# Kernel tuning notes

Measured on AMD Instinct MI355X. Metric: run time of the kernel, lower is better.

Reference implementation:

```python
import jax, jax.numpy as jnp
import numpy as np

N, D, H, HID, QK, V, PSI_HID, OUT = 100000, 128, 8, 256, 64, 64, 256, 128


def _p(key, shape, fan_in):
    return jax.random.normal(key, shape, dtype=jnp.float32) / np.sqrt(fan_in)


def setup_inputs() -> dict:
    key = jax.random.key(0)
    ks = jax.random.split(key, 16)
    coordinates = jax.random.normal(ks[0], (N, D), dtype=jnp.float32)
    mask = jnp.ones((N,), dtype=jnp.float32)
    inp = {"coordinates": coordinates, "mask": mask}
    # per-head 2-layer MLPs for q, k, v, stacked along head axis
    for name, outd, k0, k1 in (("q", QK, 1, 2), ("k", QK, 3, 4), ("v", V, 5, 6)):
        inp[f"W{name}0"] = _p(ks[k0], (H, D, HID), D)
        inp[f"b{name}0"] = jnp.zeros((H, HID), dtype=jnp.float32)
        inp[f"W{name}1"] = _p(ks[k1], (H, HID, outd), HID)
        inp[f"b{name}1"] = jnp.zeros((H, outd), dtype=jnp.float32)
    # psi MLP: concat(H*V) -> PSI_HID -> OUT
    inp["Wp0"] = _p(ks[7], (H * V, PSI_HID), H * V)
    inp["bp0"] = jnp.zeros((PSI_HID,), dtype=jnp.float32)
    inp["Wp1"] = _p(ks[8], (PSI_HID, OUT), PSI_HID)
    inp["bp1"] = jnp.zeros((OUT,), dtype=jnp.float32)
    return inp


def _mlp_heads(x, W0, b0, W1, b1):
    # x: [N, D]; W0: [H, D, M]; W1: [H, M, O] -> [H, N, O]
    h = jax.nn.relu(jnp.einsum("nd,hdm->hnm", x, W0) + b0[:, None, :])
    return jnp.einsum("hnm,hmo->hno", h, W1) + b1[:, None, :]


def _phi(x):
    return jax.nn.elu(x) + 1.0  # positive kernel feature map


def reference(coordinates, mask, Wq0, bq0, Wq1, bq1, Wk0, bk0, Wk1, bk1,
              Wv0, bv0, Wv1, bv1, Wp0, bp0, Wp1, bp1):
    m = mask[None, :, None]
    q = _mlp_heads(coordinates, Wq0, bq0, Wq1, bq1) * m  # [H, N, QK]
    k = _mlp_heads(coordinates, Wk0, bk0, Wk1, bk1) * m  # [H, N, QK]
    v = _mlp_heads(coordinates, Wv0, bv0, Wv1, bv1) * m  # [H, N, V]
    qk = _phi(q)
    kk = _phi(k)
    kv = jnp.einsum("hnk,hnv->hkv", kk, v)          # global phi(K)^T V
    sum_k = jnp.sum(kk, axis=1)                      # [H, QK]
    num = jnp.einsum("hnk,hkv->hnv", qk, kv)         # [H, N, V]
    den = jnp.einsum("hnk,hk->hn", qk, sum_k)[..., None]
    den = jnp.where(den == 0, 1e-6, den)
    heads = num / den                                # [H, N, V]
    cat = jnp.transpose(heads, (1, 0, 2)).reshape(coordinates.shape[0], -1)
    h = jax.nn.relu(cat @ Wp0 + bp0)
    out = (h @ Wp1 + bp1) * mask[:, None]
    return out
```

## Files before the change

kernel.cpp:

```cpp
#include <hip/hip_runtime.h>
#include <hip/hip_bf16.h>
#include <math.h>

#define NPTS 100000
#define NPAD 100352
#define NHALF 50176
#define RPB 3136
#define HIDST 40
#define KVST 264

typedef __bf16 bf16x8 __attribute__((ext_vector_type(8)));
typedef __bf16 bf16x4 __attribute__((ext_vector_type(4)));
typedef float f32x4 __attribute__((ext_vector_type(4)));

#define MFMA16(a,b,c) __builtin_amdgcn_mfma_f32_16x16x32_bf16((a),(b),(c),0,0,0)
#define SW(row) (((row)&7)<<3)

__global__ void k_prep_w(const float* __restrict__ Wq0, const float* __restrict__ Wk0,
                         const float* __restrict__ Wv0, const float* __restrict__ Wq1,
                         const float* __restrict__ Wk1, const float* __restrict__ Wv1,
                         const float* __restrict__ Wp0, const float* __restrict__ Wp1,
                         __bf16* __restrict__ W0t, __bf16* __restrict__ W1t,
                         __bf16* __restrict__ Wp0t, __bf16* __restrict__ Wp1t) {
  for (int i = blockIdx.x * 256 + threadIdx.x; i < 1343488; i += gridDim.x * 256) {
    if (i < 786432) {
      int g = i >> 15, j = i & 32767;
      int mat = g >> 3, h = g & 7, mcol = j >> 7, k = j & 127;
      const float* src = (mat == 0) ? Wq0 : (mat == 1) ? Wk0 : Wv0;
      W0t[i] = (__bf16)src[h * 32768 + k * 256 + mcol];
    } else if (i < 1179648) {
      int t = i - 786432;
      int g = t >> 14, j = t & 16383;
      int mat = g >> 3, h = g & 7, ocol = j >> 8, k = j & 255;
      const float* src = (mat == 0) ? Wq1 : (mat == 1) ? Wk1 : Wv1;
      W1t[t] = (__bf16)src[h * 16384 + k * 64 + ocol];
    } else if (i < 1310720) {
      int t = i - 1179648;
      int col = t >> 9, k = t & 511;
      Wp0t[t] = (__bf16)Wp0[k * 256 + col];
    } else {
      int t = i - 1310720;
      int col = t >> 8, k = t & 255;
      Wp1t[t] = (__bf16)Wp1[k * 128 + col];
    }
  }
}

__device__ __forceinline__ void load_ax(const float* __restrict__ coords,
                                        int base, int l15, int lg, bf16x8 (&ax)[4][4]) {
  #pragma unroll
  for (int jt = 0; jt < 4; ++jt) {
    int row = base + jt * 16 + l15;
    bool ok = row < NPTS;
    #pragma unroll
    for (int ks = 0; ks < 4; ++ks) {
      bf16x8 v = {};
      if (ok) {
        const float4* p4 = (const float4*)(coords + (size_t)row * 128 + ks * 32 + lg * 8);
        float4 f0 = p4[0], f1 = p4[1];
        v[0] = (__bf16)f0.x; v[1] = (__bf16)f0.y; v[2] = (__bf16)f0.z; v[3] = (__bf16)f0.w;
        v[4] = (__bf16)f1.x; v[5] = (__bf16)f1.y; v[6] = (__bf16)f1.z; v[7] = (__bf16)f1.w;
      }
      ax[jt][ks] = v;
    }
  }
}

__global__ __launch_bounds__(512, 2) void k_qgemm(
    const float* __restrict__ coords, const float* __restrict__ mask,
    const __bf16* __restrict__ W0t, const __bf16* __restrict__ W1t,
    const float* __restrict__ bq0, const float* __restrict__ bq1,
    __bf16* __restrict__ qk_ws)
{
  __shared__ __bf16 sW0[32768];
  __shared__ __bf16 sW1[16384];
  __shared__ __bf16 sHid[8 * 64 * HIDST];

  const int tid = threadIdx.x, w = tid >> 6, lane = tid & 63;
  const int l15 = lane & 15, lg = lane >> 4;
  const int h = blockIdx.x >> 5, rb = blockIdx.x & 31;

  const __bf16* w0 = W0t + (size_t)h * 32768;
  const __bf16* w1 = W1t + (size_t)h * 16384;
  #pragma unroll
  for (int i = 0; i < 8; ++i) {
    int u = tid + i * 512, row = u >> 4, k8 = (u & 15) << 3;
    *(bf16x8*)&sW0[(row * 128 + k8) ^ SW(row)] = *(const bf16x8*)(w0 + row * 128 + k8);
  }
  #pragma unroll
  for (int i = 0; i < 4; ++i) {
    int u = tid + i * 512, o = u >> 5, k8 = (u & 31) << 3;
    *(bf16x8*)&sW1[(o * 256 + k8) ^ SW(o)] = *(const bf16x8*)(w1 + o * 256 + k8);
  }
  __syncthreads();

  __bf16* myHid = sHid + w * (64 * HIDST);

  #pragma unroll 1
  for (int it = 0; it < 7; ++it) {
    const int roff = it * 512 + w * 64;
    if (roff >= RPB) break;
    const int base = rb * RPB + roff;

    bf16x8 ax[4][4];
    load_ax(coords, base, l15, lg, ax);

    f32x4 acc2[16];
    #pragma unroll
    for (int i = 0; i < 16; ++i) acc2[i] = f32x4{0.f, 0.f, 0.f, 0.f};

    #pragma unroll 1
    for (int c = 0; c < 8; ++c) {
      f32x4 a1[2][4] = {};
      #pragma unroll
      for (int ks = 0; ks < 4; ++ks) {
        bf16x8 wa[2];
        #pragma unroll
        for (int fi = 0; fi < 2; ++fi) {
          int hl = c * 32 + fi * 16 + l15;
          wa[fi] = *(const bf16x8*)&sW0[(hl * 128 + ks * 32 + lg * 8) ^ SW(hl)];
        }
        #pragma unroll
        for (int fi = 0; fi < 2; ++fi)
          #pragma unroll
          for (int jt = 0; jt < 4; ++jt)
            a1[fi][jt] = MFMA16(wa[fi], ax[jt][ks], a1[fi][jt]);
      }
      #pragma unroll
      for (int fi = 0; fi < 2; ++fi) {
        f32x4 b0v = *(const f32x4*)&bq0[h * 256 + c * 32 + fi * 16 + lg * 4];
        #pragma unroll
        for (int jt = 0; jt < 4; ++jt) {
          bf16x4 hv;
          #pragma unroll
          for (int r = 0; r < 4; ++r) {
            float v = a1[fi][jt][r] + b0v[r];
            hv[r] = (__bf16)(v > 0.f ? v : 0.f);
          }
          *(bf16x4*)&myHid[(jt * 16 + l15) * HIDST + fi * 16 + lg * 4] = hv;
        }
      }
      bf16x8 hb[4], wf[4];
      #pragma unroll
      for (int jt = 0; jt < 4; ++jt)
        hb[jt] = *(const bf16x8*)&myHid[(jt * 16 + l15) * HIDST + lg * 8];
      #pragma unroll
      for (int f = 0; f < 4; ++f) {
        int o = f * 16 + l15;
        wf[f] = *(const bf16x8*)&sW1[(o * 256 + c * 32 + lg * 8) ^ SW(o)];
      }
      #pragma unroll
      for (int ft = 0; ft < 4; ++ft)
        #pragma unroll
        for (int jt = 0; jt < 4; ++jt)
          acc2[ft * 4 + jt] = MFMA16(wf[ft], hb[jt], acc2[ft * 4 + jt]);
    }

    float mq[4];
    #pragma unroll
    for (int jt = 0; jt < 4; ++jt) {
      int rq = base + jt * 16 + l15;
      mq[jt] = (rq < NPTS) ? mask[rq] : 0.f;
    }
    #pragma unroll
    for (int ft = 0; ft < 4; ++ft) {
      f32x4 b1v = *(const f32x4*)&bq1[h * 64 + ft * 16 + lg * 4];
      #pragma unroll
      for (int jt = 0; jt < 4; ++jt) {
        bf16x4 qv;
        f32x4 a = acc2[ft * 4 + jt];
        #pragma unroll
        for (int r = 0; r < 4; ++r) {
          float v = (a[r] + b1v[r]) * mq[jt];
          qv[r] = (__bf16)(v > 0.f ? v + 1.f : __expf(v));
        }
        *(bf16x4*)(qk_ws + ((size_t)h * NPAD + base + jt * 16 + l15) * 64 + ft * 16 + lg * 4) = qv;
      }
    }
  }
}

__global__ __launch_bounds__(512, 2) void k_kvgemm(
    const float* __restrict__ coords, const float* __restrict__ mask,
    const __bf16* __restrict__ W0t, const __bf16* __restrict__ W1t,
    const float* __restrict__ bk0, const float* __restrict__ bk1,
    const float* __restrict__ bv0, const float* __restrict__ bv1,
    __bf16* __restrict__ kkTh, __bf16* __restrict__ vTh, int rowOff)
{
  __shared__ __bf16 sW0[32768];
  __shared__ __bf16 sW1[16384];
  __shared__ __bf16 sHid[8 * 64 * HIDST];

  const int tid = threadIdx.x, w = tid >> 6, lane = tid & 63;
  const int l15 = lane & 15, lg = lane >> 4;
  const int mh2 = blockIdx.x >> 4, rb = blockIdx.x & 15;
  const int m2 = mh2 >> 3, h = mh2 & 7;

  const __bf16* w0 = W0t + (size_t)((m2 + 1) * 8 + h) * 32768;
  const __bf16* w1 = W1t + (size_t)((m2 + 1) * 8 + h) * 16384;
  #pragma unroll
  for (int i = 0; i < 8; ++i) {
    int u = tid + i * 512, row = u >> 4, k8 = (u & 15) << 3;
    *(bf16x8*)&sW0[(row * 128 + k8) ^ SW(row)] = *(const bf16x8*)(w0 + row * 128 + k8);
  }
  #pragma unroll
  for (int i = 0; i < 4; ++i) {
    int u = tid + i * 512, o = u >> 5, k8 = (u & 31) << 3;
    *(bf16x8*)&sW1[(o * 256 + k8) ^ SW(o)] = *(const bf16x8*)(w1 + o * 256 + k8);
  }
  __syncthreads();

  const float* b0 = m2 ? bv0 : bk0;
  const float* b1 = m2 ? bv1 : bk1;
  __bf16* dstT = m2 ? vTh : kkTh;
  __bf16* myHid = sHid + w * (64 * HIDST);

  #pragma unroll 1
  for (int it = 0; it < 7; ++it) {
    const int roff = it * 512 + w * 64;
    if (roff >= RPB) break;
    const int lbase = rb * RPB + roff;
    const int gbase = rowOff + lbase;

    bf16x8 ax[4][4];
    load_ax(coords, gbase, l15, lg, ax);

    f32x4 acc2[16];
    #pragma unroll
    for (int i = 0; i < 16; ++i) acc2[i] = f32x4{0.f, 0.f, 0.f, 0.f};

    #pragma unroll 1
    for (int c = 0; c < 8; ++c) {
      f32x4 a1[2][4] = {};
      #pragma unroll
      for (int ks = 0; ks < 4; ++ks) {
        bf16x8 wa[2];
        #pragma unroll
        for (int fi = 0; fi < 2; ++fi) {
          int hl = c * 32 + fi * 16 + l15;
          wa[fi] = *(const bf16x8*)&sW0[(hl * 128 + ks * 32 + lg * 8) ^ SW(hl)];
        }
        #pragma unroll
        for (int fi = 0; fi < 2; ++fi)
          #pragma unroll
          for (int jt = 0; jt < 4; ++jt)
            a1[fi][jt] = MFMA16(wa[fi], ax[jt][ks], a1[fi][jt]);
      }
      #pragma unroll
      for (int fi = 0; fi < 2; ++fi) {
        f32x4 b0v = *(const f32x4*)&b0[h * 256 + c * 32 + fi * 16 + lg * 4];
        #pragma unroll
        for (int jt = 0; jt < 4; ++jt) {
          bf16x4 hv;
          #pragma unroll
          for (int r = 0; r < 4; ++r) {
            float v = a1[fi][jt][r] + b0v[r];
            hv[r] = (__bf16)(v > 0.f ? v : 0.f);
          }
          *(bf16x4*)&myHid[(jt * 16 + l15) * HIDST + fi * 16 + lg * 4] = hv;
        }
      }
      bf16x8 hb[4], wf[4];
      #pragma unroll
      for (int jt = 0; jt < 4; ++jt)
        hb[jt] = *(const bf16x8*)&myHid[(jt * 16 + l15) * HIDST + lg * 8];
      #pragma unroll
      for (int f = 0; f < 4; ++f) {
        int o = f * 16 + l15;
        wf[f] = *(const bf16x8*)&sW1[(o * 256 + c * 32 + lg * 8) ^ SW(o)];
      }
      #pragma unroll
      for (int jt = 0; jt < 4; ++jt)
        #pragma unroll
        for (int f = 0; f < 4; ++f)
          acc2[jt * 4 + f] = MFMA16(hb[jt], wf[f], acc2[jt * 4 + f]);
    }

    f32x4 mv[4];
    #pragma unroll
    for (int jt = 0; jt < 4; ++jt) {
      int rv = gbase + jt * 16 + lg * 4;
      #pragma unroll
      for (int r = 0; r < 4; ++r) mv[jt][r] = (rv + r < NPTS) ? mask[rv + r] : 0.f;
    }
    if (m2 == 0) {
      #pragma unroll
      for (int f = 0; f < 4; ++f) {
        float b1s = b1[h * 64 + f * 16 + l15];
        #pragma unroll
        for (int jt = 0; jt < 4; ++jt) {
          bf16x4 k4;
          f32x4 a = acc2[jt * 4 + f];
          #pragma unroll
          for (int r = 0; r < 4; ++r) {
            int row = gbase + jt * 16 + lg * 4 + r;
            float v = (a[r] + b1s) * mv[jt][r];
            k4[r] = (__bf16)((row < NPTS) ? (v > 0.f ? v + 1.f : __expf(v)) : 0.f);
          }
          *(bf16x4*)(dstT + (size_t)(h * 64 + f * 16 + l15) * NHALF + lbase + jt * 16 + lg * 4) = k4;
        }
      }
    } else {
      #pragma unroll
      for (int f = 0; f < 4; ++f) {
        float b1s = b1[h * 64 + f * 16 + l15];
        #pragma unroll
        for (int jt = 0; jt < 4; ++jt) {
          bf16x4 v4;
          f32x4 a = acc2[jt * 4 + f];
          #pragma unroll
          for (int r = 0; r < 4; ++r)
            v4[r] = (__bf16)((a[r] + b1s) * mv[jt][r]);
          *(bf16x4*)(dstT + (size_t)(h * 64 + f * 16 + l15) * NHALF + lbase + jt * 16 + lg * 4) = v4;
        }
      }
    }
  }
}

__global__ __launch_bounds__(256) void k_kv(
    const __bf16* __restrict__ kkTh, const __bf16* __restrict__ vTh,
    float* __restrict__ parts_kv, float* __restrict__ parts_sk, int poff)
{
  __shared__ __bf16 sA[64 * KVST];
  __shared__ __bf16 sB[64 * KVST];
  const int tid = threadIdx.x, w = tid >> 6, lane = tid & 63;
  const int l15 = lane & 15, lg = lane >> 4;
  const int sp = blockIdx.x, h = blockIdx.y;
  const int kbase0 = sp * 1024;

  bf16x8 ones;
  #pragma unroll
  for (int e = 0; e < 8; ++e) ones[e] = (__bf16)1.0f;

  f32x4 akv[4] = {};
  f32x4 ask = {};

  #pragma unroll 1
  for (int ch = 0; ch < 4; ++ch) {
    int kb = kbase0 + ch * 256;
    __syncthreads();
    #pragma unroll
    for (int i = 0; i < 8; ++i) {
      int u = tid + i * 256, row = u >> 5, k8 = (u & 31) << 3;
      *(bf16x8*)&sA[row * KVST + k8] = *(const bf16x8*)(kkTh + (size_t)(h * 64 + row) * NHALF + kb + k8);
    }
    #pragma unroll
    for (int i = 0; i < 8; ++i) {
      int u = tid + i * 256, row = u >> 5, k8 = (u & 31) << 3;
      *(bf16x8*)&sB[row * KVST + k8] = *(const bf16x8*)(vTh + (size_t)(h * 64 + row) * NHALF + kb + k8);
    }
    __syncthreads();
    #pragma unroll
    for (int ks = 0; ks < 8; ++ks) {
      bf16x8 a = *(const bf16x8*)&sA[(w * 16 + l15) * KVST + ks * 32 + lg * 8];
      #pragma unroll
      for (int fj = 0; fj < 4; ++fj) {
        bf16x8 b = *(const bf16x8*)&sB[(fj * 16 + l15) * KVST + ks * 32 + lg * 8];
        akv[fj] = MFMA16(a, b, akv[fj]);
      }
      ask = MFMA16(a, ones, ask);
    }
  }
  float* dkv = parts_kv + ((size_t)h * 98 + poff + sp) * 4096;
  #pragma unroll
  for (int fj = 0; fj < 4; ++fj)
    #pragma unroll
    for (int r = 0; r < 4; ++r)
      dkv[(size_t)(w * 16 + lg * 4 + r) * 64 + fj * 16 + l15] = akv[fj][r];
  if (l15 == 0) {
    float* dsk = parts_sk + ((size_t)h * 98 + poff + sp) * 64;
    #pragma unroll
    for (int r = 0; r < 4; ++r) dsk[w * 16 + lg * 4 + r] = ask[r];
  }
}

__global__ void k_kvt(const float* __restrict__ parts_kv, const float* __restrict__ parts_sk,
                      __bf16* __restrict__ kvTe, float* __restrict__ sumk) {
  int i = blockIdx.x * 256 + threadIdx.x;
  if (i < 32768) {
    int h = i >> 12, rem = i & 4095;
    float s = 0.f;
    for (int sp = 0; sp < 98; ++sp) s += parts_kv[((size_t)h * 98 + sp) * 4096 + rem];
    int kq = rem >> 6, j = rem & 63;
    kvTe[((size_t)h * 64 + j) * 64 + kq] = (__bf16)s;
  } else if (i < 33280) {
    int t = i - 32768;
    int h = t >> 6, c = t & 63;
    float s = 0.f;
    for (int sp = 0; sp < 98; ++sp) s += parts_sk[((size_t)h * 98 + sp) * 64 + c];
    sumk[t] = s;
  }
}

__global__ __launch_bounds__(512, 2) void k_cd(
    const float* __restrict__ mask, const __bf16* __restrict__ qk_ws,
    const __bf16* __restrict__ kvTe, const float* __restrict__ sumk,
    const __bf16* __restrict__ Wp0t, const __bf16* __restrict__ Wp1t,
    const float* __restrict__ bp0, const float* __restrict__ bp1,
    float* __restrict__ out)
{
  __shared__ __bf16 sWp0c[16384];
  __shared__ __bf16 sCat[8192];
  __shared__ __bf16 sH2[32768];
  __shared__ float sSumk[512];

  const int tid = threadIdx.x, w = tid >> 6, lane = tid & 63, l15 = lane & 15, lg = lane >> 4;
  const int rbase = blockIdx.x * 128 + w * 16;
  __bf16* myCat = sCat + w * 1024;
  __bf16* myH2 = sH2 + w * 4096;

  sSumk[tid] = sumk[tid];

  f32x4 acc1[16] = {};
  for (int h = 0; h < 8; ++h) {
    __syncthreads();
    #pragma unroll
    for (int i = 0; i < 4; ++i) {
      int u = tid + i * 512;
      int col = u >> 3, koff = (u & 7) << 3;
      *(bf16x8*)&sWp0c[(col * 64 + koff) ^ SW(col)] =
          *(const bf16x8*)(Wp0t + (size_t)col * 512 + h * 64 + koff);
    }
    __syncthreads();
    bf16x8 axq[2];
    #pragma unroll
    for (int ks = 0; ks < 2; ++ks)
      axq[ks] = *(const bf16x8*)(qk_ws + ((size_t)h * NPAD + rbase + l15) * 64 + ks * 32 + lg * 8);
    f32x4 accn[4] = {};
    #pragma unroll
    for (int ks = 0; ks < 2; ++ks)
      #pragma unroll
      for (int f = 0; f < 4; ++f) {
        bf16x8 bv = *(const bf16x8*)(kvTe + ((size_t)h * 64 + f * 16 + l15) * 64 + ks * 32 + lg * 8);
        accn[f] = MFMA16(axq[ks], bv, accn[f]);
      }
    float p = 0.f;
    #pragma unroll
    for (int ks = 0; ks < 2; ++ks)
      #pragma unroll
      for (int e = 0; e < 8; ++e)
        p += (float)axq[ks][e] * sSumk[h * 64 + ks * 32 + lg * 8 + e];
    p += __shfl_xor(p, 16);
    p += __shfl_xor(p, 32);
    float dinv[4];
    #pragma unroll
    for (int r = 0; r < 4; ++r) {
      float d = __shfl(p, (lane & 48) + ((lane >> 4) << 2) + r);
      d = (d == 0.f) ? 1e-6f : d;
      dinv[r] = 1.f / d;
    }
    #pragma unroll
    for (int f = 0; f < 4; ++f)
      #pragma unroll
      for (int r = 0; r < 4; ++r) {
        int row = lg * 4 + r;
        myCat[(row * 64 + f * 16 + l15) ^ SW(row)] = (__bf16)(accn[f][r] * dinv[r]);
      }
    #pragma unroll
    for (int ks2 = 0; ks2 < 2; ++ks2) {
      bf16x8 aC = *(const bf16x8*)&myCat[(l15 * 64 + ks2 * 32 + lg * 8) ^ SW(l15)];
      #pragma unroll
      for (int f = 0; f < 16; ++f) {
        bf16x8 bw = *(const bf16x8*)&sWp0c[((f * 16 + l15) * 64 + ks2 * 32 + lg * 8) ^ SW(l15)];
        acc1[f] = MFMA16(aC, bw, acc1[f]);
      }
    }
  }
  #pragma unroll
  for (int f = 0; f < 16; ++f) {
    float bias = bp0[f * 16 + l15];
    #pragma unroll
    for (int r = 0; r < 4; ++r) {
      int row = lg * 4 + r;
      float val = acc1[f][r] + bias;
      val = val > 0.f ? val : 0.f;
      myH2[(row * 256 + f * 16 + l15) ^ SW(row)] = (__bf16)val;
    }
  }
  f32x4 acc2[8] = {};
  #pragma unroll
  for (int ks = 0; ks < 8; ++ks) {
    bf16x8 aH = *(const bf16x8*)&myH2[(l15 * 256 + ks * 32 + lg * 8) ^ SW(l15)];
    #pragma unroll
    for (int f = 0; f < 8; ++f) {
      bf16x8 bw = *(const bf16x8*)(Wp1t + (size_t)(f * 16 + l15) * 256 + ks * 32 + lg * 8);
      acc2[f] = MFMA16(aH, bw, acc2[f]);
    }
  }
  float mvr[4];
  #pragma unroll
  for (int r = 0; r < 4; ++r) {
    int grow = rbase + lg * 4 + r;
    mvr[r] = (grow < NPTS) ? mask[grow] : 0.f;
  }
  #pragma unroll
  for (int f = 0; f < 8; ++f) {
    int col = f * 16 + l15;
    float bias = bp1[col];
    #pragma unroll
    for (int r = 0; r < 4; ++r) {
      int grow = rbase + lg * 4 + r;
      if (grow < NPTS) out[(size_t)grow * 128 + col] = (acc2[f][r] + bias) * mvr[r];
    }
  }
}

extern "C" void kernel_launch(void* const* d_in, const int* in_sizes, int n_in,
                              void* d_out, int out_size, void* d_ws, size_t ws_size,
                              hipStream_t stream) {
  const float* coords = (const float*)d_in[0];
  const float* mask   = (const float*)d_in[1];
  const float* Wq0 = (const float*)d_in[2];
  const float* bq0 = (const float*)d_in[3];
  const float* Wq1 = (const float*)d_in[4];
  const float* bq1 = (const float*)d_in[5];
  const float* Wk0 = (const float*)d_in[6];
  const float* bk0 = (const float*)d_in[7];
  const float* Wk1 = (const float*)d_in[8];
  const float* bk1 = (const float*)d_in[9];
  const float* Wv0 = (const float*)d_in[10];
  const float* bv0 = (const float*)d_in[11];
  const float* Wv1 = (const float*)d_in[12];
  const float* bv1 = (const float*)d_in[13];
  const float* Wp0 = (const float*)d_in[14];
  const float* bp0 = (const float*)d_in[15];
  const float* Wp1 = (const float*)d_in[16];
  const float* bp1 = (const float*)d_in[17];
  float* out = (float*)d_out;

  char* p = (char*)d_ws;
  __bf16* region0  = (__bf16*)p; p += (size_t)8 * NPAD * 64 * 2;
  __bf16* qk_ws    = region0;
  __bf16* kkTh     = region0;
  __bf16* vTh      = region0 + (size_t)8 * 64 * NHALF;
  __bf16* W0t      = (__bf16*)p; p += (size_t)24 * 32768 * 2;
  __bf16* W1t      = (__bf16*)p; p += (size_t)24 * 16384 * 2;
  __bf16* Wp0t     = (__bf16*)p; p += (size_t)256 * 512 * 2;
  __bf16* Wp1t     = (__bf16*)p; p += (size_t)128 * 256 * 2;
  float*  parts_kv = (float*)p;  p += (size_t)8 * 98 * 4096 * 4;
  float*  parts_sk = (float*)p;  p += (size_t)8 * 98 * 64 * 4;
  float*  sumk     = (float*)p;  p += (size_t)512 * 4;
  __bf16* kvTe     = (__bf16*)p; p += (size_t)8 * 64 * 64 * 2;

  k_prep_w<<<1024, 256, 0, stream>>>(Wq0, Wk0, Wv0, Wq1, Wk1, Wv1, Wp0, Wp1,
                                     W0t, W1t, Wp0t, Wp1t);
  k_kvgemm<<<256, 512, 0, stream>>>(coords, mask, W0t, W1t, bk0, bk1, bv0, bv1,
                                    kkTh, vTh, 0);
  k_kv<<<dim3(49, 8), 256, 0, stream>>>(kkTh, vTh, parts_kv, parts_sk, 0);
  k_kvgemm<<<256, 512, 0, stream>>>(coords, mask, W0t, W1t, bk0, bk1, bv0, bv1,
                                    kkTh, vTh, NHALF);
  k_kv<<<dim3(49, 8), 256, 0, stream>>>(kkTh, vTh, parts_kv, parts_sk, 49);
  k_qgemm<<<256, 512, 0, stream>>>(coords, mask, W0t, W1t, bq0, bq1, qk_ws);
  k_kvt<<<130, 256, 0, stream>>>(parts_kv, parts_sk, kvTe, sumk);
  k_cd<<<784, 512, 0, stream>>>(mask, qk_ws, kvTe, sumk, Wp0t, Wp1t, bp0, bp1, out);
}
```

Before: 591.7 us.

## Read Wp0 directly from global in k_cd, drop staging and barriers, chunk second GEMM

The k_cd kernel no longer stages the per-head Wp0 slice into shared memory with two block barriers per head. Each wave now reads the Wp0 fragments straight from global/L2. The hidden-layer epilogue is processed in four 64-column chunks through a small padded per-wave buffer instead of a full 256-wide H2 tile. This cuts LDS use from about 114KB to about 36KB, which could allow more blocks per CU and removes block-wide synchronisation, at the cost of more global/L2 traffic for the weight reads. The swizzled layouts are also replaced with padded strides (68).

```diff
diff --git a/kernel.cpp b/kernel.cpp
--- a/kernel.cpp
+++ b/kernel.cpp
@@ -8,6 +8,7 @@
 #define RPB 3136
 #define HIDST 40
 #define KVST 264
+#define CDST 68
 
 typedef __bf16 bf16x8 __attribute__((ext_vector_type(8)));
 typedef __bf16 bf16x4 __attribute__((ext_vector_type(4)));
@@ -400,29 +401,21 @@
     const float* __restrict__ bp0, const float* __restrict__ bp1,
     float* __restrict__ out)
 {
-  __shared__ __bf16 sWp0c[16384];
-  __shared__ __bf16 sCat[8192];
-  __shared__ __bf16 sH2[32768];
+  __shared__ __bf16 sCat[8 * 16 * CDST];
+  __shared__ __bf16 sHc[8 * 16 * CDST];
   __shared__ float sSumk[512];
 
   const int tid = threadIdx.x, w = tid >> 6, lane = tid & 63, l15 = lane & 15, lg = lane >> 4;
   const int rbase = blockIdx.x * 128 + w * 16;
-  __bf16* myCat = sCat + w * 1024;
-  __bf16* myH2 = sH2 + w * 4096;
+  __bf16* myCat = sCat + w * (16 * CDST);
+  __bf16* myHc = sHc + w * (16 * CDST);
 
   sSumk[tid] = sumk[tid];
+  __syncthreads();
 
   f32x4 acc1[16] = {};
+  #pragma unroll 1
   for (int h = 0; h < 8; ++h) {
-    __syncthreads();
-    #pragma unroll
-    for (int i = 0; i < 4; ++i) {
-      int u = tid + i * 512;
-      int col = u >> 3, koff = (u & 7) << 3;
-      *(bf16x8*)&sWp0c[(col * 64 + koff) ^ SW(col)] =
-          *(const bf16x8*)(Wp0t + (size_t)col * 512 + h * 64 + koff);
-    }
-    __syncthreads();
     bf16x8 axq[2];
     #pragma unroll
     for (int ks = 0; ks < 2; ++ks)
@@ -453,39 +446,39 @@
     #pragma unroll
     for (int f = 0; f < 4; ++f)
       #pragma unroll
+      for (int r = 0; r < 4; ++r)
+        myCat[(lg * 4 + r) * CDST + f * 16 + l15] = (__bf16)(accn[f][r] * dinv[r]);
+    #pragma unroll
+    for (int ks2 = 0; ks2 < 2; ++ks2) {
+      bf16x8 aC = *(const bf16x8*)&myCat[l15 * CDST + ks2 * 32 + lg * 8];
+      #pragma unroll
+      for (int f = 0; f < 16; ++f) {
+        bf16x8 bw = *(const bf16x8*)(Wp0t + (size_t)(f * 16 + l15) * 512 + h * 64 + ks2 * 32 + lg * 8);
+        acc1[f] = MFMA16(aC, bw, acc1[f]);
+      }
+    }
+  }
+  f32x4 acc2[8] = {};
+  #pragma unroll 1
+  for (int c = 0; c < 4; ++c) {
+    #pragma unroll
+    for (int fi = 0; fi < 4; ++fi) {
+      float bias = bp0[(c * 4 + fi) * 16 + l15];
+      #pragma unroll
       for (int r = 0; r < 4; ++r) {
-        int row = lg * 4 + r;
-        myCat[(row * 64 + f * 16 + l15) ^ SW(row)] = (__bf16)(accn[f][r] * dinv[r]);
-      }
+        float val = acc1[c * 4 + fi][r] + bias;
+        val = val > 0.f ? val : 0.f;
+        myHc[(lg * 4 + r) * CDST + fi * 16 + l15] = (__bf16)val;
+      }
+    }
     #pragma unroll
     for (int ks2 = 0; ks2 < 2; ++ks2) {
-      bf16x8 aC = *(const bf16x8*)&myCat[(l15 * 64 + ks2 * 32 + lg * 8) ^ SW(l15)];
-      #pragma unroll
-      for (int f = 0; f < 16; ++f) {
-        bf16x8 bw = *(const bf16x8*)&sWp0c[((f * 16 + l15) * 64 + ks2 * 32 + lg * 8) ^ SW(l15)];
-        acc1[f] = MFMA16(aC, bw, acc1[f]);
-      }
-    }
-  }
-  #pragma unroll
-  for (int f = 0; f < 16; ++f) {
-    float bias = bp0[f * 16 + l15];
-    #pragma unroll
-    for (int r = 0; r < 4; ++r) {
-      int row = lg * 4 + r;
-      float val = acc1[f][r] + bias;
-      val = val > 0.f ? val : 0.f;
-      myH2[(row * 256 + f * 16 + l15) ^ SW(row)] = (__bf16)val;
-    }
-  }
-  f32x4 acc2[8] = {};
-  #pragma unroll
-  for (int ks = 0; ks < 8; ++ks) {
-    bf16x8 aH = *(const bf16x8*)&myH2[(l15 * 256 + ks * 32 + lg * 8) ^ SW(l15)];
-    #pragma unroll
-    for (int f = 0; f < 8; ++f) {
-      bf16x8 bw = *(const bf16x8*)(Wp1t + (size_t)(f * 16 + l15) * 256 + ks * 32 + lg * 8);
-      acc2[f] = MFMA16(aH, bw, acc2[f]);
+      bf16x8 aH = *(const bf16x8*)&myHc[l15 * CDST + ks2 * 32 + lg * 8];
+      #pragma unroll
+      for (int f = 0; f < 8; ++f) {
+        bf16x8 bw = *(const bf16x8*)(Wp1t + (size_t)(f * 16 + l15) * 256 + c * 64 + ks2 * 32 + lg * 8);
+        acc2[f] = MFMA16(aH, bw, acc2[f]);
+      }
     }
   }
   float mvr[4];
```

New measurement: 825.7 us. 39.5% more time.
